# Kernel optimization log

Hardware: AMD Instinct MI355X
Metric: run time of the kernel (lower is better)

Reference implementation:

```python
import jax, jax.numpy as jnp
import numpy as np

L, H, D = 4, 8, 256  # layers, heads, feature dim (Z has d+1 = 257 channels)
B, N1 = 8, 2048      # batch, N+1 tokens (N = 2047 context + 1 query)
STD = 0.02


def setup_inputs() -> dict:
    key = jax.random.key(0)
    k1, k2 = jax.random.split(key)
    Z = jax.random.normal(k1, (B, N1, D + 1), dtype=jnp.float32)
    allparam = STD * jax.random.normal(k2, (L, H, 2, D, D), dtype=jnp.float32)
    return {"Z": Z, "allparam": allparam}


def _attention(P, Q, Z):
    # P, Q: (d, d); Z: (B, N+1, d+1). act is None -> purely bilinear.
    Bn, N1_, d1 = Z.shape
    N, d = N1_ - 1, d1 - 1
    # Zero-padded (d+1, d+1) versions: P_full has a 1 in the label corner.
    P_full = jnp.zeros((d + 1, d + 1), Z.dtype).at[:d, :d].set(P).at[d, d].set(1.0)
    Q_full = jnp.zeros((d + 1, d + 1), Z.dtype).at[:d, :d].set(Q)
    sim = jnp.einsum('BNi,ij,BMj->BNM', Z, Q_full, Z)   # (B, N+1, N+1)
    val = jnp.einsum('ij,BNj->BNi', P_full, Z)            # (B, N+1, d+1)
    # A = eye(N+1) with A[N, N] = 0  ->  sim @ A @ val == sim @ (val with last token zeroed)
    val = val.at[:, N, :].set(0.0)
    return jnp.einsum('BNM,BMi->BNi', sim, val) / N


def reference(Z, allparam):
    for i in range(L):
        res = 0.0
        for j in range(H):  # small fixed head loop, matches torch structure
            P = allparam[i, j, 0]
            Q = allparam[i, j, 1]
            res = res + _attention(P, Q, Z)
        Z = Z + res
    return Z
```

## Files before the change

kernel.cpp:

```cpp
#include <hip/hip_runtime.h>


#define NL   4
#define NH   8
#define DD   256
#define NCH  257
#define NTOK 2048
#define NVAL 2047
#define NB   8

typedef short  short8v __attribute__((ext_vector_type(8)));
typedef short  short4v __attribute__((ext_vector_type(4)));
typedef float  f32x4   __attribute__((ext_vector_type(4)));

__device__ __forceinline__ unsigned short f2b(float x) {
  union { float f; unsigned u; } v; v.f = x;
  unsigned u = v.u + 0x7fffu + ((v.u >> 16) & 1u);
  return (unsigned short)(u >> 16);
}
__device__ __forceinline__ float b2f(short s) {
  union { unsigned u; float f; } v; v.u = ((unsigned)(unsigned short)s) << 16;
  return v.f;
}

__device__ __forceinline__ void mm_tile(const short* __restrict__ A, const short* __restrict__ B,
                                        int lda, int ldb, int ar, int bc, int k0, int k1,
                                        int lane, f32x4 acc[4][4]) {
  #pragma unroll 2
  for (int kk = k0; kk < k1; kk += 32) {
    const int kc = kk + ((lane >> 4) << 3);
    short8v av[4], bv[4];
    #pragma unroll
    for (int f = 0; f < 4; ++f)
      av[f] = *(const short8v*)(A + (size_t)(ar + f * 16 + (lane & 15)) * lda + kc);
    #pragma unroll
    for (int g = 0; g < 4; ++g)
      bv[g] = *(const short8v*)(B + (size_t)(bc + g * 16 + (lane & 15)) * ldb + kc);
    #pragma unroll
    for (int f = 0; f < 4; ++f)
      #pragma unroll
      for (int g = 0; g < 4; ++g)
        acc[f][g] = __builtin_amdgcn_mfma_f32_16x16x32_bf16(av[f], bv[g], acc[f][g], 0, 0, 0);
  }
}

__global__ __launch_bounds__(256) void k_prep_pq(const float* __restrict__ ap,
                                                 short* __restrict__ Pbf, short* __restrict__ Qbf) {
  int gid = blockIdx.x * 256 + threadIdx.x;
  int lj = gid >> 14, rc4 = gid & 16383;
  const f32x4* src = (const f32x4*)ap;
  f32x4 pv = src[(size_t)(lj * 2 + 0) * 16384 + rc4];
  f32x4 qv = src[(size_t)(lj * 2 + 1) * 16384 + rc4];
  short4v p, q;
  #pragma unroll
  for (int i = 0; i < 4; ++i) { p[i] = (short)f2b(pv[i]); q[i] = (short)f2b(qv[i]); }
  ((short4v*)Pbf)[(size_t)lj * 16384 + rc4] = p;
  ((short4v*)Qbf)[(size_t)lj * 16384 + rc4] = q;
}

__global__ __launch_bounds__(256) void k_qsumt(const float* __restrict__ ap, float* __restrict__ QsumT) {
  __shared__ float lds[64][65];
  const int l = blockIdx.y;
  const int k0 = (blockIdx.x >> 2) * 64, t0 = (blockIdx.x & 3) * 64;
  const int tid = threadIdx.x, c = tid & 63, r = tid >> 6;
  #pragma unroll
  for (int i = 0; i < 16; ++i) {
    int k = r + i * 4;
    float s = 0.f;
    #pragma unroll
    for (int j = 0; j < 8; ++j)
      s += ap[(size_t)((l * 8 + j) * 2 + 1) * 65536 + (size_t)(k0 + k) * 256 + (t0 + c)];
    lds[k][c] = s;
  }
  __syncthreads();
  #pragma unroll
  for (int i = 0; i < 16; ++i) {
    int tl = r + i * 4;
    QsumT[(size_t)l * 65536 + (size_t)(t0 + tl) * 256 + (k0 + c)] = lds[c][tl];
  }
}

__global__ __launch_bounds__(256) void k_transpose(const float* __restrict__ Z,
                                                   short* __restrict__ Zxt, short* __restrict__ Zxbf,
                                                   float* __restrict__ gcol) {
  __shared__ float tile[64][65];
  __shared__ float zl[64];
  const int k0 = blockIdx.x * 64, m0 = blockIdx.y * 64, b = blockIdx.z;
  const int tid = threadIdx.x, c = tid & 63, r = tid >> 6;
  #pragma unroll
  for (int i = 0; i < 16; ++i) {
    int mrow = r + i * 4, m = m0 + mrow;
    float v = Z[((size_t)b * NTOK + m) * NCH + k0 + c];
    tile[mrow][c] = v;
    Zxbf[((size_t)b * NTOK + m) * DD + k0 + c] = (short)f2b(v);
  }
  if (tid < 64) {
    int m = m0 + tid;
    zl[tid] = (m == NVAL) ? 0.f : Z[((size_t)b * NTOK + m) * NCH + DD];
  }
  __syncthreads();
  #pragma unroll
  for (int i = 0; i < 16; ++i) {
    int krow = r + i * 4;
    float v = tile[c][krow];
    if (m0 + c == NVAL) v = 0.f;
    Zxt[((size_t)b * DD + k0 + krow) * NTOK + m0 + c] = (short)f2b(v);
  }
  float s = 0.f;
  #pragma unroll
  for (int i = 0; i < 16; ++i) s += tile[r * 16 + i][c] * zl[r * 16 + i];
  atomicAdd(&gcol[b * 256 + k0 + c], s);
}

__global__ __launch_bounds__(256) void k_gram(const short* __restrict__ Zxt, float* __restrict__ Gacc) {
  const int tid = threadIdx.x, lane = tid & 63, wid = tid >> 6;
  const int wr = wid >> 1, wc = wid & 1;
  const int seg = blockIdx.y, b = blockIdx.z;
  const int ar = (blockIdx.x >> 1) * 128 + wr * 64;
  const int bc = (blockIdx.x & 1) * 128 + wc * 64;
  const short* A = Zxt + (size_t)b * DD * NTOK;
  f32x4 acc[4][4];
  #pragma unroll
  for (int f = 0; f < 4; ++f) for (int g = 0; g < 4; ++g) for (int i = 0; i < 4; ++i) acc[f][g][i] = 0.f;
  mm_tile(A, A, NTOK, NTOK, ar, bc, seg * 256, seg * 256 + 256, lane, acc);
  float* out = Gacc + (size_t)(seg * 8 + b) * 65536;
  #pragma unroll
  for (int f = 0; f < 4; ++f)
    #pragma unroll
    for (int g = 0; g < 4; ++g)
      #pragma unroll
      for (int i = 0; i < 4; ++i)
        out[(size_t)(ar + f * 16 + ((lane >> 4) << 2) + i) * 256 + bc + g * 16 + (lane & 15)] = acc[f][g][i];
}

__global__ __launch_bounds__(256) void k_gconv(const float* __restrict__ Gacc, short* __restrict__ Gbf) {
  const int b = blockIdx.x >> 5, t = blockIdx.x & 31;
  const int e0 = t * 2048 + threadIdx.x * 8;
  float a[8];
  #pragma unroll
  for (int i = 0; i < 8; ++i) a[i] = 0.f;
  #pragma unroll
  for (int s = 0; s < 8; ++s) {
    const f32x4* p = (const f32x4*)(Gacc + (size_t)(s * 8 + b) * 65536 + e0);
    f32x4 x = p[0], y = p[1];
    #pragma unroll
    for (int i = 0; i < 4; ++i) { a[i] += x[i]; a[4 + i] += y[i]; }
  }
  short8v o;
  #pragma unroll
  for (int i = 0; i < 8; ++i) o[i] = (short)f2b(a[i]);
  *(short8v*)(Gbf + (size_t)b * 65536 + e0) = o;
}

__global__ __launch_bounds__(256) void k_pmul(const short* __restrict__ Gbf, const short* __restrict__ Pbf,
                                              short* __restrict__ Vt, int layer) {
  const int tid = threadIdx.x, lane = tid & 63, wid = tid >> 6;
  const int wr = wid >> 1, wc = wid & 1;
  const int j = blockIdx.y, b = blockIdx.z;
  const int ar = (blockIdx.x >> 1) * 128 + wr * 64;
  const int bc = (blockIdx.x & 1) * 128 + wc * 64;
  const short* A = Gbf + (size_t)b * 65536;
  const short* B = Pbf + (size_t)(layer * 8 + j) * 65536;
  f32x4 acc[4][4];
  #pragma unroll
  for (int f = 0; f < 4; ++f) for (int g = 0; g < 4; ++g) for (int i = 0; i < 4; ++i) acc[f][g][i] = 0.f;
  mm_tile(A, B, 256, 256, ar, bc, 0, 256, lane, acc);
  short* out = Vt + (size_t)(b * 8 + j) * 65536;
  #pragma unroll
  for (int f = 0; f < 4; ++f)
    #pragma unroll
    for (int g = 0; g < 4; ++g) {
      int c = bc + g * 16 + (lane & 15);
      int t0 = ar + f * 16 + ((lane >> 4) << 2);
      short4v p;
      #pragma unroll
      for (int i = 0; i < 4; ++i) p[i] = (short)f2b(acc[f][g][i]);
      *(short4v*)(out + (size_t)c * 256 + t0) = p;
    }
}

__global__ __launch_bounds__(256) void k_qmul(const short* __restrict__ Qbf, const short* __restrict__ Vt,
                                              float* __restrict__ Macc, int layer) {
  const int tid = threadIdx.x, lane = tid & 63, wid = tid >> 6;
  const int wr = wid >> 1, wc = wid & 1;
  const int jseg = blockIdx.y, b = blockIdx.z;
  const int ar = (blockIdx.x >> 1) * 128 + wr * 64;
  const int bc = (blockIdx.x & 1) * 128 + wc * 64;
  f32x4 acc[4][4];
  #pragma unroll
  for (int f = 0; f < 4; ++f) for (int g = 0; g < 4; ++g) for (int i = 0; i < 4; ++i) acc[f][g][i] = 0.f;
  for (int jj = jseg * 2; jj < jseg * 2 + 2; ++jj) {
    const short* A = Qbf + (size_t)(layer * 8 + jj) * 65536;
    const short* B = Vt + (size_t)(b * 8 + jj) * 65536;
    mm_tile(A, B, 256, 256, ar, bc, 0, 256, lane, acc);
  }
  float* out = Macc + (size_t)(jseg * 8 + b) * 65536;
  #pragma unroll
  for (int f = 0; f < 4; ++f)
    #pragma unroll
    for (int g = 0; g < 4; ++g)
      #pragma unroll
      for (int i = 0; i < 4; ++i)
        out[(size_t)(ar + f * 16 + ((lane >> 4) << 2) + i) * 256 + bc + g * 16 + (lane & 15)] = acc[f][g][i];
}

__global__ __launch_bounds__(256) void k_mconv(const float* __restrict__ Macc, short* __restrict__ Mt,
                                               const float* __restrict__ QsumT, const float* __restrict__ gcol,
                                               float* __restrict__ mcol, int layer) {
  const float invN = 1.0f / (float)NVAL;
  const int b = blockIdx.y, tid = threadIdx.x;
  if (blockIdx.x == 16) {
    __shared__ float gs[256];
    gs[tid] = gcol[b * 256 + tid];
    __syncthreads();
    float s = 0.f;
    for (int t = 0; t < 256; ++t) s += QsumT[(size_t)layer * 65536 + (size_t)t * 256 + tid] * gs[t];
    mcol[b * 256 + tid] = s * invN;
    return;
  }
  __shared__ float lds[64][65];
  const int k0 = (blockIdx.x >> 2) * 64, c0 = (blockIdx.x & 3) * 64;
  const int c = tid & 63, r = tid >> 6;
  #pragma unroll
  for (int i = 0; i < 16; ++i) {
    int k = r + i * 4;
    float s = 0.f;
    #pragma unroll
    for (int p = 0; p < 4; ++p)
      s += Macc[(size_t)(p * 8 + b) * 65536 + (size_t)(k0 + k) * 256 + c0 + c];
    lds[k][c] = s * invN;
  }
  __syncthreads();
  #pragma unroll
  for (int i = 0; i < 16; ++i) {
    int cl = r + i * 4;
    Mt[(size_t)b * 65536 + (size_t)(c0 + cl) * 256 + (k0 + c)] = (short)f2b(lds[c][cl]);
  }
}

__global__ __launch_bounds__(256) void k_apply(float* __restrict__ Z,
                                               const short* __restrict__ Zxbf, const short* __restrict__ Mt,
                                               const float* __restrict__ mcol, float* __restrict__ gcol) {
  const int tid = threadIdx.x, lane = tid & 63, wid = tid >> 6;
  const int wr = wid >> 1, wc = wid & 1;
  const int b = blockIdx.z;
  const int ar = blockIdx.y * 128 + wr * 64;
  const int bc = blockIdx.x * 128 + wc * 64;
  if (blockIdx.x == 0 && blockIdx.y == 0) gcol[b * 256 + tid] = 0.f;
  const short* A = Zxbf + (size_t)b * NTOK * DD;
  const short* B = Mt + (size_t)b * 65536;
  const bool gemv = (blockIdx.x == 0 && wc == 0);
  f32x4 acc[4][4];
  #pragma unroll
  for (int f = 0; f < 4; ++f) for (int g = 0; g < 4; ++g) for (int i = 0; i < 4; ++i) acc[f][g][i] = 0.f;
  float s[4] = {0.f, 0.f, 0.f, 0.f};
  #pragma unroll 2
  for (int kk = 0; kk < 256; kk += 32) {
    const int kc = kk + ((lane >> 4) << 3);
    short8v av[4], bv[4];
    #pragma unroll
    for (int f = 0; f < 4; ++f)
      av[f] = *(const short8v*)(A + (size_t)(ar + f * 16 + (lane & 15)) * DD + kc);
    #pragma unroll
    for (int g = 0; g < 4; ++g)
      bv[g] = *(const short8v*)(B + (size_t)(bc + g * 16 + (lane & 15)) * 256 + kc);
    if (gemv) {
      const float* mp = mcol + b * 256 + kc;
      f32x4 m0 = *(const f32x4*)mp, m1 = *(const f32x4*)(mp + 4);
      #pragma unroll
      for (int f = 0; f < 4; ++f) {
        #pragma unroll
        for (int q = 0; q < 4; ++q) {
          s[f] += b2f(av[f][q]) * m0[q];
          s[f] += b2f(av[f][4 + q]) * m1[q];
        }
      }
    }
    #pragma unroll
    for (int f = 0; f < 4; ++f)
      #pragma unroll
      for (int g = 0; g < 4; ++g)
        acc[f][g] = __builtin_amdgcn_mfma_f32_16x16x32_bf16(av[f], bv[g], acc[f][g], 0, 0, 0);
  }
  #pragma unroll
  for (int f = 0; f < 4; ++f)
    #pragma unroll
    for (int g = 0; g < 4; ++g)
      #pragma unroll
      for (int i = 0; i < 4; ++i) {
        int n = ar + f * 16 + ((lane >> 4) << 2) + i;
        int c = bc + g * 16 + (lane & 15);
        size_t idx = ((size_t)b * NTOK + n) * NCH + c;
        Z[idx] += acc[f][g][i];
      }
  if (gemv) {
    #pragma unroll
    for (int f = 0; f < 4; ++f) {
      float t = s[f];
      t += __shfl_xor(t, 16);
      t += __shfl_xor(t, 32);
      if ((lane >> 4) == 0) {
        int n = ar + f * 16 + (lane & 15);
        Z[((size_t)b * NTOK + n) * NCH + DD] += t;
      }
    }
  }
}

__global__ __launch_bounds__(256) void gram_kernel(const float* __restrict__ Z, float* __restrict__ G) {
  __shared__ float As[32][64];
  __shared__ float Bs[32][65];
  const int c0 = blockIdx.x * 64, k0 = blockIdx.y * 64, b = blockIdx.z;
  const int tid = threadIdx.x, tx = tid & 15, ty = tid >> 4;
  const float* Zb = Z + (size_t)b * NTOK * NCH;
  float acc[4][4] = {};
  for (int m0 = 0; m0 < NVAL; m0 += 32) {
    #pragma unroll
    for (int l = 0; l < 8; ++l) {
      int e = tid + l * 256, mm = e >> 6, kk = e & 63, m = m0 + mm;
      As[mm][kk] = (m < NVAL) ? Zb[(size_t)m * NCH + (k0 + kk)] : 0.f;
    }
    #pragma unroll
    for (int l = 0; l < 8; ++l) {
      int e = tid + l * 256, mm = e >> 6, cc = e & 63, m = m0 + mm, c = c0 + cc;
      Bs[mm][cc] = (m < NVAL && c < NCH) ? Zb[(size_t)m * NCH + c] : 0.f;
    }
    __syncthreads();
    #pragma unroll
    for (int mm = 0; mm < 32; ++mm) {
      float a[4], bb[4];
      #pragma unroll
      for (int i = 0; i < 4; ++i) a[i] = As[mm][ty * 4 + i];
      #pragma unroll
      for (int j = 0; j < 4; ++j) bb[j] = Bs[mm][tx * 4 + j];
      #pragma unroll
      for (int i = 0; i < 4; ++i)
        #pragma unroll
        for (int j = 0; j < 4; ++j) acc[i][j] += a[i] * bb[j];
    }
    __syncthreads();
  }
  float* Gb = G + (size_t)b * DD * NCH;
  #pragma unroll
  for (int i = 0; i < 4; ++i) {
    int k = k0 + ty * 4 + i;
    #pragma unroll
    for (int j = 0; j < 4; ++j) {
      int c = c0 + tx * 4 + j;
      if (c < NCH) Gb[(size_t)k * NCH + c] = acc[i][j];
    }
  }
}
__global__ __launch_bounds__(256) void pmul_kernel(const float* __restrict__ G, const float* __restrict__ allparam,
                                                   float* __restrict__ U, int layer, int j0, int JB) {
  __shared__ float As[64][33];
  __shared__ float Bs[64][33];
  const int c0 = blockIdx.x * 64, k0 = blockIdx.y * 64;
  const int b = blockIdx.z / JB, jj = blockIdx.z % JB, j = j0 + jj;
  const int tid = threadIdx.x, tx = tid & 15, ty = tid >> 4;
  const float* P = allparam + ((size_t)((layer * NH + j) * 2 + 0)) * DD * DD;
  const float* Gb = G + (size_t)b * DD * NCH;
  float acc[4][4] = {};
  for (int t0 = 0; t0 < DD; t0 += 32) {
    #pragma unroll
    for (int l = 0; l < 8; ++l) {
      int e = tid + l * 256, kk = e >> 5, tt = e & 31;
      As[kk][tt] = Gb[(size_t)(k0 + kk) * NCH + (t0 + tt)];
    }
    #pragma unroll
    for (int l = 0; l < 8; ++l) {
      int e = tid + l * 256, cc = e >> 5, tt = e & 31, c = c0 + cc;
      Bs[cc][tt] = (c < DD) ? P[(size_t)c * DD + (t0 + tt)] : 0.f;
    }
    __syncthreads();
    #pragma unroll
    for (int tt = 0; tt < 32; ++tt) {
      float a[4], bb[4];
      #pragma unroll
      for (int i = 0; i < 4; ++i) a[i] = As[ty * 4 + i][tt];
      #pragma unroll
      for (int j2 = 0; j2 < 4; ++j2) bb[j2] = Bs[tx * 4 + j2][tt];
      #pragma unroll
      for (int i = 0; i < 4; ++i)
        #pragma unroll
        for (int j2 = 0; j2 < 4; ++j2) acc[i][j2] += a[i] * bb[j2];
    }
    __syncthreads();
  }
  float* Us = U + ((size_t)(b * JB + jj)) * DD * NCH;
  #pragma unroll
  for (int i = 0; i < 4; ++i) {
    int k = k0 + ty * 4 + i;
    #pragma unroll
    for (int j2 = 0; j2 < 4; ++j2) {
      int c = c0 + tx * 4 + j2;
      if (c < DD)       Us[(size_t)k * NCH + c] = acc[i][j2];
      else if (c == DD) Us[(size_t)k * NCH + c] = Gb[(size_t)k * NCH + DD];
    }
  }
}
__global__ __launch_bounds__(256) void qmul_kernel(const float* __restrict__ U, const float* __restrict__ allparam,
                                                   float* __restrict__ M, int layer, int j0, int jcount, int JB,
                                                   int accumulate) {
  __shared__ float As[64][33];
  __shared__ float Bs[32][65];
  const int c0 = blockIdx.x * 64, k0 = blockIdx.y * 64, b = blockIdx.z;
  const int tid = threadIdx.x, tx = tid & 15, ty = tid >> 4;
  const float invN = 1.0f / (float)NVAL;
  float acc[4][4] = {};
  for (int jj = 0; jj < jcount; ++jj) {
    const float* Q = allparam + ((size_t)((layer * NH + (j0 + jj)) * 2 + 1)) * DD * DD;
    const float* Ub = U + ((size_t)(b * JB + jj)) * DD * NCH;
    for (int t0 = 0; t0 < DD; t0 += 32) {
      #pragma unroll
      for (int l = 0; l < 8; ++l) {
        int e = tid + l * 256, kk = e >> 5, tt = e & 31;
        As[kk][tt] = Q[(size_t)(k0 + kk) * DD + (t0 + tt)];
      }
      #pragma unroll
      for (int l = 0; l < 8; ++l) {
        int e = tid + l * 256, tt = e >> 6, cc = e & 63, c = c0 + cc;
        Bs[tt][cc] = (c < NCH) ? Ub[(size_t)(t0 + tt) * NCH + c] : 0.f;
      }
      __syncthreads();
      #pragma unroll
      for (int tt = 0; tt < 32; ++tt) {
        float a[4], bb[4];
        #pragma unroll
        for (int i = 0; i < 4; ++i) a[i] = As[ty * 4 + i][tt];
        #pragma unroll
        for (int j2 = 0; j2 < 4; ++j2) bb[j2] = Bs[tt][tx * 4 + j2];
        #pragma unroll
        for (int i = 0; i < 4; ++i)
          #pragma unroll
          for (int j2 = 0; j2 < 4; ++j2) acc[i][j2] += a[i] * bb[j2];
      }
      __syncthreads();
    }
  }
  #pragma unroll
  for (int i = 0; i < 4; ++i) {
    int k = k0 + ty * 4 + i;
    #pragma unroll
    for (int j2 = 0; j2 < 4; ++j2) {
      int c = c0 + tx * 4 + j2;
      if (c < NCH) {
        size_t idx = ((size_t)b * DD + k) * NCH + c;
        float v = invN * acc[i][j2];
        M[idx] = accumulate ? (M[idx] + v) : v;
      }
    }
  }
}
__global__ __launch_bounds__(256) void apply_kernel(float* __restrict__ Z, const float* __restrict__ M) {
  __shared__ float Zs[8][256];
  const int b = blockIdx.y, n0 = blockIdx.x * 8;
  float* Zb = Z + (size_t)b * NTOK * NCH;
  const float* Mb = M + (size_t)b * DD * NCH;
  const int tid = threadIdx.x;
  #pragma unroll
  for (int l = 0; l < 8; ++l) {
    int e = tid + l * 256, r = e >> 8, k = e & 255;
    Zs[r][k] = Zb[(size_t)(n0 + r) * NCH + k];
  }
  __syncthreads();
  const int r = tid >> 5, cbase = tid & 31;
  float acc[9] = {};
  #pragma unroll 4
  for (int k = 0; k < 256; ++k) {
    float z = Zs[r][k];
    const float* Mrow = Mb + (size_t)k * NCH;
    #pragma unroll
    for (int ii = 0; ii < 8; ++ii) acc[ii] += z * Mrow[cbase + ii * 32];
    if (cbase == 0) acc[8] += z * Mrow[256];
  }
  #pragma unroll
  for (int ii = 0; ii < 8; ++ii)
    Zb[(size_t)(n0 + r) * NCH + cbase + ii * 32] += acc[ii];
  if (cbase == 0) Zb[(size_t)(n0 + r) * NCH + 256] += acc[8];
}

extern "C" void kernel_launch(void* const* d_in, const int* in_sizes, int n_in,
                              void* d_out, int out_size, void* d_ws, size_t ws_size,
                              hipStream_t stream) {
  const float* Zin      = (const float*)d_in[0];
  const float* allparam = (const float*)d_in[1];
  float* Z = (float*)d_out;
  const size_t zbytes = (size_t)NB * NTOK * NCH * sizeof(float);

  const size_t o_zxbf = 0;
  const size_t o_zxt  = o_zxbf + 8388608;
  const size_t o_gacc = o_zxt  + 8388608;
  const size_t o_gbf  = o_gacc + 16777216;
  const size_t o_vt   = o_gbf  + 1048576;
  const size_t o_mt   = o_vt   + 8388608;
  const size_t o_pbf  = o_mt   + 1048576;
  const size_t o_qbf  = o_pbf  + 4194304;
  const size_t o_qsum = o_qbf  + 4194304;
  const size_t o_gcol = o_qsum + 1048576;
  const size_t o_mcol = o_gcol + 8192;
  const size_t NEED   = o_mcol + 8192;

  if (ws_size >= NEED) {
    char* wsb = (char*)d_ws;
    short* Zxbf = (short*)(wsb + o_zxbf);
    short* Zxt  = (short*)(wsb + o_zxt);
    float* Gacc = (float*)(wsb + o_gacc);
    float* Macc = Gacc;
    short* Gbf  = (short*)(wsb + o_gbf);
    short* Vt   = (short*)(wsb + o_vt);
    short* Mt   = (short*)(wsb + o_mt);
    short* Pbf  = (short*)(wsb + o_pbf);
    short* Qbf  = (short*)(wsb + o_qbf);
    float* QsumT= (float*)(wsb + o_qsum);
    float* gcol = (float*)(wsb + o_gcol);
    float* mcol = (float*)(wsb + o_mcol);

    hipMemcpyAsync(Z, Zin, zbytes, hipMemcpyDeviceToDevice, stream);
    hipMemsetAsync(gcol, 0, 8192, stream);
    k_prep_pq<<<dim3(2048), dim3(256), 0, stream>>>(allparam, Pbf, Qbf);
    k_qsumt<<<dim3(16, 4), dim3(256), 0, stream>>>(allparam, QsumT);

    for (int layer = 0; layer < NL; ++layer) {
      k_transpose<<<dim3(4, 32, NB), dim3(256), 0, stream>>>(Z, Zxt, Zxbf, gcol);
      k_gram<<<dim3(4, 8, NB), dim3(256), 0, stream>>>(Zxt, Gacc);
      k_gconv<<<dim3(256), dim3(256), 0, stream>>>(Gacc, Gbf);
      k_pmul<<<dim3(4, 8, NB), dim3(256), 0, stream>>>(Gbf, Pbf, Vt, layer);
      k_qmul<<<dim3(4, 4, NB), dim3(256), 0, stream>>>(Qbf, Vt, Macc, layer);
      k_mconv<<<dim3(17, NB), dim3(256), 0, stream>>>(Macc, Mt, QsumT, gcol, mcol, layer);
      k_apply<<<dim3(2, 16, NB), dim3(256), 0, stream>>>(Z, Zxbf, Mt, mcol, gcol);
    }
    return;
  }

  hipMemcpyAsync(Z, Zin, zbytes, hipMemcpyDeviceToDevice, stream);
  const size_t Gn = (size_t)NB * DD * NCH;
  float* ws   = (float*)d_ws;
  float* Gbuf = ws;
  float* Mbuf = ws + Gn;
  float* Ubuf = ws + 2 * Gn;
  const int JB = (ws_size >= (size_t)(2 + 8) * Gn * sizeof(float)) ? 8 : 1;
  dim3 blk(256);
  for (int layer = 0; layer < NL; ++layer) {
    gram_kernel<<<dim3(5, 4, NB), blk, 0, stream>>>(Z, Gbuf);
    for (int j0 = 0; j0 < NH; j0 += JB) {
      pmul_kernel<<<dim3(5, 4, NB * JB), blk, 0, stream>>>(Gbuf, allparam, Ubuf, layer, j0, JB);
      qmul_kernel<<<dim3(5, 4, NB), blk, 0, stream>>>(Ubuf, allparam, Mbuf, layer, j0, JB, JB,
                                                      (j0 == 0) ? 0 : 1);
    }
    apply_kernel<<<dim3(NTOK / 8, NB), blk, 0, stream>>>(Z, Mbuf);
  }
}
```

Before: 387.0 us.

## Fuse init kernels, drop split-K gram/M reductions, emit next-layer bf16 copies from apply

The separate P/Q conversion, Q-sum and first transpose kernels are merged into one init kernel that reads the input directly, so the device-to-device copy is no longer needed. The gram kernel now runs the full K range per block and computes only the upper block-triangle, mirroring the off-diagonal tile. The label-column product moves into a dedicated block of that kernel, and the fp32 split-K buffer and its conversion kernel are removed. The Q·V product and the M conversion are fused into one kernel that accumulates all heads and writes bf16 directly. The apply kernel writes the next layer's bf16 row-major and transposed Z and the label column, which replaces the per-layer transpose kernel. These changes cut launches and intermediate traffic, but the gram and M GEMMs now run on far fewer blocks, and the transposed writes from apply are scattered.

```diff
diff --git a/kernel.cpp b/kernel.cpp
--- a/kernel.cpp
+++ b/kernel.cpp
@@ -23,7 +23,7 @@
   return v.f;
 }
 
-__device__ __forceinline__ void mm_tile(const short* __restrict__ A, const short* __restrict__ B,
+__device__ __forceinline__ void mm_tile(const short* A, const short* B,
                                         int lda, int ldb, int ar, int bc, int k0, int k1,
                                         int lane, f32x4 acc[4][4]) {
   #pragma unroll 2
@@ -44,112 +44,120 @@
   }
 }
 
-__global__ __launch_bounds__(256) void k_prep_pq(const float* __restrict__ ap,
-                                                 short* __restrict__ Pbf, short* __restrict__ Qbf) {
-  int gid = blockIdx.x * 256 + threadIdx.x;
-  int lj = gid >> 14, rc4 = gid & 16383;
-  const f32x4* src = (const f32x4*)ap;
-  f32x4 pv = src[(size_t)(lj * 2 + 0) * 16384 + rc4];
-  f32x4 qv = src[(size_t)(lj * 2 + 1) * 16384 + rc4];
-  short4v p, q;
-  #pragma unroll
-  for (int i = 0; i < 4; ++i) { p[i] = (short)f2b(pv[i]); q[i] = (short)f2b(qv[i]); }
-  ((short4v*)Pbf)[(size_t)lj * 16384 + rc4] = p;
-  ((short4v*)Qbf)[(size_t)lj * 16384 + rc4] = q;
-}
-
-__global__ __launch_bounds__(256) void k_qsumt(const float* __restrict__ ap, float* __restrict__ QsumT) {
+__global__ __launch_bounds__(256) void k_init(const float* __restrict__ Zin,
+                                              const float* __restrict__ ap,
+                                              short* __restrict__ Pbf, short* __restrict__ Qbf,
+                                              float* __restrict__ QsumT,
+                                              short* __restrict__ Zxbf, short* __restrict__ Zxt,
+                                              float* __restrict__ zlab) {
   __shared__ float lds[64][65];
-  const int l = blockIdx.y;
-  const int k0 = (blockIdx.x >> 2) * 64, t0 = (blockIdx.x & 3) * 64;
-  const int tid = threadIdx.x, c = tid & 63, r = tid >> 6;
-  #pragma unroll
-  for (int i = 0; i < 16; ++i) {
-    int k = r + i * 4;
-    float s = 0.f;
-    #pragma unroll
-    for (int j = 0; j < 8; ++j)
-      s += ap[(size_t)((l * 8 + j) * 2 + 1) * 65536 + (size_t)(k0 + k) * 256 + (t0 + c)];
-    lds[k][c] = s;
-  }
-  __syncthreads();
-  #pragma unroll
-  for (int i = 0; i < 16; ++i) {
-    int tl = r + i * 4;
-    QsumT[(size_t)l * 65536 + (size_t)(t0 + tl) * 256 + (k0 + c)] = lds[c][tl];
-  }
-}
-
-__global__ __launch_bounds__(256) void k_transpose(const float* __restrict__ Z,
-                                                   short* __restrict__ Zxt, short* __restrict__ Zxbf,
-                                                   float* __restrict__ gcol) {
-  __shared__ float tile[64][65];
-  __shared__ float zl[64];
-  const int k0 = blockIdx.x * 64, m0 = blockIdx.y * 64, b = blockIdx.z;
-  const int tid = threadIdx.x, c = tid & 63, r = tid >> 6;
+  const int bx = blockIdx.x, tid = threadIdx.x;
+  if (bx < 2048) {
+    int gid = bx * 256 + tid;
+    int lj = gid >> 14, rc4 = gid & 16383;
+    const f32x4* src = (const f32x4*)ap;
+    f32x4 pv = src[(size_t)(lj * 2 + 0) * 16384 + rc4];
+    f32x4 qv = src[(size_t)(lj * 2 + 1) * 16384 + rc4];
+    short4v p, q;
+    #pragma unroll
+    for (int i = 0; i < 4; ++i) { p[i] = (short)f2b(pv[i]); q[i] = (short)f2b(qv[i]); }
+    ((short4v*)Pbf)[(size_t)lj * 16384 + rc4] = p;
+    ((short4v*)Qbf)[(size_t)lj * 16384 + rc4] = q;
+    return;
+  }
+  if (bx < 2112) {
+    int qb = bx - 2048;
+    int l = qb >> 4, xx = qb & 15;
+    int k0 = (xx >> 2) * 64, t0 = (xx & 3) * 64;
+    int c = tid & 63, r = tid >> 6;
+    #pragma unroll
+    for (int i = 0; i < 16; ++i) {
+      int k = r + i * 4;
+      float s = 0.f;
+      #pragma unroll
+      for (int j = 0; j < 8; ++j)
+        s += ap[(size_t)((l * 8 + j) * 2 + 1) * 65536 + (size_t)(k0 + k) * 256 + (t0 + c)];
+      lds[k][c] = s;
+    }
+    __syncthreads();
+    #pragma unroll
+    for (int i = 0; i < 16; ++i) {
+      int tl = r + i * 4;
+      QsumT[(size_t)l * 65536 + (size_t)(t0 + tl) * 256 + (k0 + c)] = lds[c][tl];
+    }
+    return;
+  }
+  int tb = bx - 2112;
+  int x = tb & 3, y = (tb >> 2) & 31, b = tb >> 7;
+  int k0 = x * 64, m0 = y * 64;
+  int c = tid & 63, r = tid >> 6;
   #pragma unroll
   for (int i = 0; i < 16; ++i) {
     int mrow = r + i * 4, m = m0 + mrow;
-    float v = Z[((size_t)b * NTOK + m) * NCH + k0 + c];
-    tile[mrow][c] = v;
+    float v = Zin[((size_t)b * NTOK + m) * NCH + k0 + c];
+    lds[mrow][c] = v;
     Zxbf[((size_t)b * NTOK + m) * DD + k0 + c] = (short)f2b(v);
   }
-  if (tid < 64) {
+  if (x == 0 && tid < 64) {
     int m = m0 + tid;
-    zl[tid] = (m == NVAL) ? 0.f : Z[((size_t)b * NTOK + m) * NCH + DD];
+    zlab[b * NTOK + m] = (m == NVAL) ? 0.f : Zin[((size_t)b * NTOK + m) * NCH + DD];
   }
   __syncthreads();
   #pragma unroll
   for (int i = 0; i < 16; ++i) {
     int krow = r + i * 4;
-    float v = tile[c][krow];
+    float v = lds[c][krow];
     if (m0 + c == NVAL) v = 0.f;
     Zxt[((size_t)b * DD + k0 + krow) * NTOK + m0 + c] = (short)f2b(v);
   }
-  float s = 0.f;
-  #pragma unroll
-  for (int i = 0; i < 16; ++i) s += tile[r * 16 + i][c] * zl[r * 16 + i];
-  atomicAdd(&gcol[b * 256 + k0 + c], s);
-}
-
-__global__ __launch_bounds__(256) void k_gram(const short* __restrict__ Zxt, float* __restrict__ Gacc) {
+}
+
+__global__ __launch_bounds__(256) void k_gram(const short* __restrict__ Zxt,
+                                              const float* __restrict__ zlab,
+                                              short* __restrict__ Gbf, float* __restrict__ gcol) {
+  const int b = blockIdx.y, x = blockIdx.x;
   const int tid = threadIdx.x, lane = tid & 63, wid = tid >> 6;
+  if (x == 3) {
+    __shared__ float zl[NTOK];
+    #pragma unroll
+    for (int i = 0; i < 8; ++i) zl[tid + i * 256] = zlab[b * NTOK + tid + i * 256];
+    __syncthreads();
+    const short* row = Zxt + ((size_t)b * DD + tid) * NTOK;
+    float s = 0.f;
+    for (int m = 0; m < NTOK; m += 8) {
+      short8v v = *(const short8v*)(row + m);
+      #pragma unroll
+      for (int q = 0; q < 8; ++q) s += b2f(v[q]) * zl[m + q];
+    }
+    gcol[b * DD + tid] = s;
+    return;
+  }
+  const int ar0 = (x == 1) ? 128 : 0;
+  const int bc0 = (x == 0) ? 0 : 128;
   const int wr = wid >> 1, wc = wid & 1;
-  const int seg = blockIdx.y, b = blockIdx.z;
-  const int ar = (blockIdx.x >> 1) * 128 + wr * 64;
-  const int bc = (blockIdx.x & 1) * 128 + wc * 64;
+  const int ar = ar0 + wr * 64, bc = bc0 + wc * 64;
   const short* A = Zxt + (size_t)b * DD * NTOK;
   f32x4 acc[4][4];
   #pragma unroll
   for (int f = 0; f < 4; ++f) for (int g = 0; g < 4; ++g) for (int i = 0; i < 4; ++i) acc[f][g][i] = 0.f;
-  mm_tile(A, A, NTOK, NTOK, ar, bc, seg * 256, seg * 256 + 256, lane, acc);
-  float* out = Gacc + (size_t)(seg * 8 + b) * 65536;
-  #pragma unroll
-  for (int f = 0; f < 4; ++f)
-    #pragma unroll
-    for (int g = 0; g < 4; ++g)
-      #pragma unroll
-      for (int i = 0; i < 4; ++i)
-        out[(size_t)(ar + f * 16 + ((lane >> 4) << 2) + i) * 256 + bc + g * 16 + (lane & 15)] = acc[f][g][i];
-}
-
-__global__ __launch_bounds__(256) void k_gconv(const float* __restrict__ Gacc, short* __restrict__ Gbf) {
-  const int b = blockIdx.x >> 5, t = blockIdx.x & 31;
-  const int e0 = t * 2048 + threadIdx.x * 8;
-  float a[8];
-  #pragma unroll
-  for (int i = 0; i < 8; ++i) a[i] = 0.f;
-  #pragma unroll
-  for (int s = 0; s < 8; ++s) {
-    const f32x4* p = (const f32x4*)(Gacc + (size_t)(s * 8 + b) * 65536 + e0);
-    f32x4 x = p[0], y = p[1];
-    #pragma unroll
-    for (int i = 0; i < 4; ++i) { a[i] += x[i]; a[4 + i] += y[i]; }
-  }
-  short8v o;
-  #pragma unroll
-  for (int i = 0; i < 8; ++i) o[i] = (short)f2b(a[i]);
-  *(short8v*)(Gbf + (size_t)b * 65536 + e0) = o;
+  mm_tile(A, A, NTOK, NTOK, ar, bc, 0, NTOK, lane, acc);
+  short* Gb = Gbf + (size_t)b * 65536;
+  #pragma unroll
+  for (int f = 0; f < 4; ++f) {
+    const int rb = ar + f * 16 + ((lane >> 4) << 2);
+    #pragma unroll
+    for (int g = 0; g < 4; ++g) {
+      const int cc = bc + g * 16 + (lane & 15);
+      short4v mv;
+      #pragma unroll
+      for (int i = 0; i < 4; ++i) {
+        unsigned short bv = f2b(acc[f][g][i]);
+        Gb[(size_t)(rb + i) * 256 + cc] = (short)bv;
+        mv[i] = (short)bv;
+      }
+      if (x == 2) *(short4v*)(Gb + (size_t)cc * 256 + rb) = mv;
+    }
+  }
 }
 
 __global__ __launch_bounds__(256) void k_pmul(const short* __restrict__ Gbf, const short* __restrict__ Pbf,
@@ -167,49 +175,25 @@
   mm_tile(A, B, 256, 256, ar, bc, 0, 256, lane, acc);
   short* out = Vt + (size_t)(b * 8 + j) * 65536;
   #pragma unroll
-  for (int f = 0; f < 4; ++f)
+  for (int f = 0; f < 4; ++f) {
+    const int t0 = ar + f * 16 + ((lane >> 4) << 2);
     #pragma unroll
     for (int g = 0; g < 4; ++g) {
-      int c = bc + g * 16 + (lane & 15);
-      int t0 = ar + f * 16 + ((lane >> 4) << 2);
+      const int c = bc + g * 16 + (lane & 15);
       short4v p;
       #pragma unroll
       for (int i = 0; i < 4; ++i) p[i] = (short)f2b(acc[f][g][i]);
       *(short4v*)(out + (size_t)c * 256 + t0) = p;
     }
-}
-
-__global__ __launch_bounds__(256) void k_qmul(const short* __restrict__ Qbf, const short* __restrict__ Vt,
-                                              float* __restrict__ Macc, int layer) {
-  const int tid = threadIdx.x, lane = tid & 63, wid = tid >> 6;
-  const int wr = wid >> 1, wc = wid & 1;
-  const int jseg = blockIdx.y, b = blockIdx.z;
-  const int ar = (blockIdx.x >> 1) * 128 + wr * 64;
-  const int bc = (blockIdx.x & 1) * 128 + wc * 64;
-  f32x4 acc[4][4];
-  #pragma unroll
-  for (int f = 0; f < 4; ++f) for (int g = 0; g < 4; ++g) for (int i = 0; i < 4; ++i) acc[f][g][i] = 0.f;
-  for (int jj = jseg * 2; jj < jseg * 2 + 2; ++jj) {
-    const short* A = Qbf + (size_t)(layer * 8 + jj) * 65536;
-    const short* B = Vt + (size_t)(b * 8 + jj) * 65536;
-    mm_tile(A, B, 256, 256, ar, bc, 0, 256, lane, acc);
-  }
-  float* out = Macc + (size_t)(jseg * 8 + b) * 65536;
-  #pragma unroll
-  for (int f = 0; f < 4; ++f)
-    #pragma unroll
-    for (int g = 0; g < 4; ++g)
-      #pragma unroll
-      for (int i = 0; i < 4; ++i)
-        out[(size_t)(ar + f * 16 + ((lane >> 4) << 2) + i) * 256 + bc + g * 16 + (lane & 15)] = acc[f][g][i];
-}
-
-__global__ __launch_bounds__(256) void k_mconv(const float* __restrict__ Macc, short* __restrict__ Mt,
-                                               const float* __restrict__ QsumT, const float* __restrict__ gcol,
-                                               float* __restrict__ mcol, int layer) {
+  }
+}
+
+__global__ __launch_bounds__(256) void k_m(const short* __restrict__ Qbf, const short* __restrict__ Vt,
+                                           const float* __restrict__ QsumT, const float* __restrict__ gcol,
+                                           short* __restrict__ Mt, float* __restrict__ mcol, int layer) {
   const float invN = 1.0f / (float)NVAL;
-  const int b = blockIdx.y, tid = threadIdx.x;
-  if (blockIdx.x == 16) {
+  const int b = blockIdx.y, x = blockIdx.x, tid = threadIdx.x;
+  if (x == 4) {
     __shared__ float gs[256];
     gs[tid] = gcol[b * 256 + tid];
     __syncthreads();
@@ -218,36 +202,42 @@
     mcol[b * 256 + tid] = s * invN;
     return;
   }
-  __shared__ float lds[64][65];
-  const int k0 = (blockIdx.x >> 2) * 64, c0 = (blockIdx.x & 3) * 64;
-  const int c = tid & 63, r = tid >> 6;
-  #pragma unroll
-  for (int i = 0; i < 16; ++i) {
-    int k = r + i * 4;
-    float s = 0.f;
-    #pragma unroll
-    for (int p = 0; p < 4; ++p)
-      s += Macc[(size_t)(p * 8 + b) * 65536 + (size_t)(k0 + k) * 256 + c0 + c];
-    lds[k][c] = s * invN;
-  }
-  __syncthreads();
-  #pragma unroll
-  for (int i = 0; i < 16; ++i) {
-    int cl = r + i * 4;
-    Mt[(size_t)b * 65536 + (size_t)(c0 + cl) * 256 + (k0 + c)] = (short)f2b(lds[c][cl]);
-  }
-}
-
-__global__ __launch_bounds__(256) void k_apply(float* __restrict__ Z,
-                                               const short* __restrict__ Zxbf, const short* __restrict__ Mt,
-                                               const float* __restrict__ mcol, float* __restrict__ gcol) {
+  const int lane = tid & 63, wid = tid >> 6;
+  const int wr = wid >> 1, wc = wid & 1;
+  const int ar = (x >> 1) * 128 + wr * 64;
+  const int bc = (x & 1) * 128 + wc * 64;
+  f32x4 acc[4][4];
+  #pragma unroll
+  for (int f = 0; f < 4; ++f) for (int g = 0; g < 4; ++g) for (int i = 0; i < 4; ++i) acc[f][g][i] = 0.f;
+  for (int j = 0; j < 8; ++j)
+    mm_tile(Qbf + (size_t)(layer * 8 + j) * 65536, Vt + (size_t)(b * 8 + j) * 65536,
+            256, 256, ar, bc, 0, 256, lane, acc);
+  short* out = Mt + (size_t)b * 65536;
+  #pragma unroll
+  for (int f = 0; f < 4; ++f) {
+    const int k0 = ar + f * 16 + ((lane >> 4) << 2);
+    #pragma unroll
+    for (int g = 0; g < 4; ++g) {
+      const int c = bc + g * 16 + (lane & 15);
+      short4v p;
+      #pragma unroll
+      for (int i = 0; i < 4; ++i) p[i] = (short)f2b(acc[f][g][i] * invN);
+      *(short4v*)(out + (size_t)c * 256 + k0) = p;
+    }
+  }
+}
+
+__global__ __launch_bounds__(256) void k_apply(const float* __restrict__ Zsrc, float* __restrict__ Z,
+                                               const short* __restrict__ Zxbf_in, const short* __restrict__ Mt,
+                                               const float* __restrict__ mcol,
+                                               short* __restrict__ Zxbf_out, short* __restrict__ Zxt_out,
+                                               float* __restrict__ zlab_out, int wnext) {
   const int tid = threadIdx.x, lane = tid & 63, wid = tid >> 6;
   const int wr = wid >> 1, wc = wid & 1;
   const int b = blockIdx.z;
   const int ar = blockIdx.y * 128 + wr * 64;
   const int bc = blockIdx.x * 128 + wc * 64;
-  if (blockIdx.x == 0 && blockIdx.y == 0) gcol[b * 256 + tid] = 0.f;
-  const short* A = Zxbf + (size_t)b * NTOK * DD;
+  const short* A = Zxbf_in + (size_t)b * NTOK * DD;
   const short* B = Mt + (size_t)b * 65536;
   const bool gemv = (blockIdx.x == 0 && wc == 0);
   f32x4 acc[4][4];
@@ -283,16 +273,24 @@
         acc[f][g] = __builtin_amdgcn_mfma_f32_16x16x32_bf16(av[f], bv[g], acc[f][g], 0, 0, 0);
   }
   #pragma unroll
-  for (int f = 0; f < 4; ++f)
-    #pragma unroll
-    for (int g = 0; g < 4; ++g)
+  for (int f = 0; f < 4; ++f) {
+    const int nb = ar + f * 16 + ((lane >> 4) << 2);
+    #pragma unroll
+    for (int g = 0; g < 4; ++g) {
+      const int c = bc + g * 16 + (lane & 15);
+      short4v tz;
       #pragma unroll
       for (int i = 0; i < 4; ++i) {
-        int n = ar + f * 16 + ((lane >> 4) << 2) + i;
-        int c = bc + g * 16 + (lane & 15);
-        size_t idx = ((size_t)b * NTOK + n) * NCH + c;
-        Z[idx] += acc[f][g][i];
-      }
+        size_t idx = ((size_t)b * NTOK + nb + i) * NCH + c;
+        float nv = Zsrc[idx] + acc[f][g][i];
+        Z[idx] = nv;
+        unsigned short bv = f2b(nv);
+        if (wnext) Zxbf_out[((size_t)b * NTOK + nb + i) * DD + c] = (short)bv;
+        tz[i] = (nb + i == NVAL) ? (short)0 : (short)bv;
+      }
+      if (wnext) *(short4v*)(Zxt_out + ((size_t)b * DD + c) * NTOK + nb) = tz;
+    }
+  }
   if (gemv) {
     #pragma unroll
     for (int f = 0; f < 4; ++f) {
@@ -301,7 +299,10 @@
       t += __shfl_xor(t, 32);
       if ((lane >> 4) == 0) {
         int n = ar + f * 16 + (lane & 15);
-        Z[((size_t)b * NTOK + n) * NCH + DD] += t;
+        size_t idx = ((size_t)b * NTOK + n) * NCH + DD;
+        float nv = Zsrc[idx] + t;
+        Z[idx] = nv;
+        if (wnext) zlab_out[b * NTOK + n] = (n == NVAL) ? 0.f : nv;
       }
     }
   }
@@ -486,12 +487,11 @@
   const float* Zin      = (const float*)d_in[0];
   const float* allparam = (const float*)d_in[1];
   float* Z = (float*)d_out;
-  const size_t zbytes = (size_t)NB * NTOK * NCH * sizeof(float);
-
-  const size_t o_zxbf = 0;
-  const size_t o_zxt  = o_zxbf + 8388608;
-  const size_t o_gacc = o_zxt  + 8388608;
-  const size_t o_gbf  = o_gacc + 16777216;
+
+  const size_t o_zx0  = 0;
+  const size_t o_zx1  = o_zx0  + 8388608;
+  const size_t o_zxt  = o_zx1  + 8388608;
+  const size_t o_gbf  = o_zxt  + 8388608;
   const size_t o_vt   = o_gbf  + 1048576;
   const size_t o_mt   = o_vt   + 8388608;
   const size_t o_pbf  = o_mt   + 1048576;
@@ -499,40 +499,39 @@
   const size_t o_qsum = o_qbf  + 4194304;
   const size_t o_gcol = o_qsum + 1048576;
   const size_t o_mcol = o_gcol + 8192;
-  const size_t NEED   = o_mcol + 8192;
+  const size_t o_zlab = o_mcol + 8192;
+  const size_t NEED   = o_zlab + 65536;
 
   if (ws_size >= NEED) {
     char* wsb = (char*)d_ws;
-    short* Zxbf = (short*)(wsb + o_zxbf);
-    short* Zxt  = (short*)(wsb + o_zxt);
-    float* Gacc = (float*)(wsb + o_gacc);
-    float* Macc = Gacc;
-    short* Gbf  = (short*)(wsb + o_gbf);
-    short* Vt   = (short*)(wsb + o_vt);
-    short* Mt   = (short*)(wsb + o_mt);
-    short* Pbf  = (short*)(wsb + o_pbf);
-    short* Qbf  = (short*)(wsb + o_qbf);
-    float* QsumT= (float*)(wsb + o_qsum);
-    float* gcol = (float*)(wsb + o_gcol);
-    float* mcol = (float*)(wsb + o_mcol);
-
-    hipMemcpyAsync(Z, Zin, zbytes, hipMemcpyDeviceToDevice, stream);
-    hipMemsetAsync(gcol, 0, 8192, stream);
-    k_prep_pq<<<dim3(2048), dim3(256), 0, stream>>>(allparam, Pbf, Qbf);
-    k_qsumt<<<dim3(16, 4), dim3(256), 0, stream>>>(allparam, QsumT);
+    short* Zx[2] = { (short*)(wsb + o_zx0), (short*)(wsb + o_zx1) };
+    short* Zxt   = (short*)(wsb + o_zxt);
+    short* Gbf   = (short*)(wsb + o_gbf);
+    short* Vt    = (short*)(wsb + o_vt);
+    short* Mt    = (short*)(wsb + o_mt);
+    short* Pbf   = (short*)(wsb + o_pbf);
+    short* Qbf   = (short*)(wsb + o_qbf);
+    float* QsumT = (float*)(wsb + o_qsum);
+    float* gcol  = (float*)(wsb + o_gcol);
+    float* mcol  = (float*)(wsb + o_mcol);
+    float* zlab  = (float*)(wsb + o_zlab);
+
+    k_init<<<dim3(3136), dim3(256), 0, stream>>>(Zin, allparam, Pbf, Qbf, QsumT, Zx[0], Zxt, zlab);
 
     for (int layer = 0; layer < NL; ++layer) {
-      k_transpose<<<dim3(4, 32, NB), dim3(256), 0, stream>>>(Z, Zxt, Zxbf, gcol);
-      k_gram<<<dim3(4, 8, NB), dim3(256), 0, stream>>>(Zxt, Gacc);
-      k_gconv<<<dim3(256), dim3(256), 0, stream>>>(Gacc, Gbf);
+      const int cur = layer & 1;
+      const int wnext = (layer < NL - 1) ? 1 : 0;
+      const float* Zsrc = (layer == 0) ? Zin : Z;
+      k_gram<<<dim3(4, NB), dim3(256), 0, stream>>>(Zxt, zlab, Gbf, gcol);
       k_pmul<<<dim3(4, 8, NB), dim3(256), 0, stream>>>(Gbf, Pbf, Vt, layer);
-      k_qmul<<<dim3(4, 4, NB), dim3(256), 0, stream>>>(Qbf, Vt, Macc, layer);
-      k_mconv<<<dim3(17, NB), dim3(256), 0, stream>>>(Macc, Mt, QsumT, gcol, mcol, layer);
-      k_apply<<<dim3(2, 16, NB), dim3(256), 0, stream>>>(Z, Zxbf, Mt, mcol, gcol);
+      k_m<<<dim3(5, NB), dim3(256), 0, stream>>>(Qbf, Vt, QsumT, gcol, Mt, mcol, layer);
+      k_apply<<<dim3(2, 16, NB), dim3(256), 0, stream>>>(Zsrc, Z, Zx[cur], Mt, mcol,
+                                                         Zx[cur ^ 1], Zxt, zlab, wnext);
     }
     return;
   }
 
+  const size_t zbytes = (size_t)NB * NTOK * NCH * sizeof(float);
   hipMemcpyAsync(Z, Zin, zbytes, hipMemcpyDeviceToDevice, stream);
   const size_t Gn = (size_t)NB * DD * NCH;
   float* ws   = (float*)d_ws;
```

Result: slower. 822.1 us (+112.4%).
